# Performance work log

Measured on AMD Instinct MI355X. Metric: run time of the kernel, lower is better.

The kernel has to match this reference:

```python
import jax, jax.numpy as jnp
import numpy as np

H = 256   # hidden_dim
K = 4     # number of z_layer Linears
T = 8192  # number of permutation trees (Z-nodes) in the batch
C = 16    # children (leaf indices) per tree
N = 200000  # rows in batch.x node-feature table


def setup_inputs() -> dict:
    key = jax.random.key(0)
    ks = jax.random.split(key, 6)
    x = jax.random.normal(ks[0], (N, H), dtype=jnp.float32)
    leaf_idx = jax.random.randint(ks[1], (T, C), 0, N)
    # z_layer: k Linears (y = x @ W + b), z_final_layer: one Linear
    scale = 1.0 / np.sqrt(H)
    Wz = jax.random.uniform(ks[2], (K, H, H), dtype=jnp.float32, minval=-scale, maxval=scale)
    bz = jax.random.uniform(ks[3], (K, H), dtype=jnp.float32, minval=-scale, maxval=scale)
    Wzf = jax.random.uniform(ks[4], (H, H), dtype=jnp.float32, minval=-scale, maxval=scale)
    bzf = jax.random.uniform(ks[5], (H,), dtype=jnp.float32, minval=-scale, maxval=scale)
    return {"x": x, "Wz": Wz, "bz": bz, "Wzf": Wzf, "bzf": bzf, "leaf_idx": leaf_idx}


def reference(x, Wz, bz, Wzf, bzf, leaf_idx):
    # Batched z_layer_fn over T trees, each a Z-node over C leaf children.
    data = x[leaf_idx]                                   # [T, C, H] gather (fetch_or_produce)
    # k parallel Linears: [K, T, C, H]
    after = jnp.einsum('tch,khd->ktcd', data, Wz) + bz[:, None, None, :]
    # embedding_k[torch.roll(arange(C), shifts=k)] == roll(embedding_k, k, axis=children)
    k = after.shape[0]
    rolled_sum = after[0]
    for i in range(1, k):  # tiny fixed loop over k layers
        rolled_sum = rolled_sum + jnp.roll(after[i], i, axis=1)
    h = jax.nn.elu(rolled_sum)                           # [T, C, H]
    h = jnp.einsum('tch,hd->tcd', h, Wzf) + bzf          # z_final_layer
    out = jax.nn.elu(jnp.sum(h, axis=1))                 # sum over children, ELU -> [T, H]
    return out
```

## Files before the change

kernel.cpp:

```cpp
#include <hip/hip_runtime.h>
#include <hip/hip_bf16.h>
#include <stdint.h>

#define TREES 8192
#define HID   256
#define CH    16
#define KL    4
#define G     8
#define LDSS  264

typedef short bf16x8 __attribute__((ext_vector_type(8)));
typedef float f32x4  __attribute__((ext_vector_type(4)));

__device__ __forceinline__ unsigned short f2bf(float f) {
    unsigned u = __builtin_bit_cast(unsigned, f);
    u += 0x7FFFu + ((u >> 16) & 1u);
    return (unsigned short)(u >> 16);
}
__device__ __forceinline__ float elu1(float x) {
    return x > 0.f ? x : (__expf(x) - 1.f);
}

__global__ void prep_transpose(const float* __restrict__ Wz,
                               const float* __restrict__ Wzf,
                               unsigned short* __restrict__ WzT,
                               unsigned short* __restrict__ WzfT) {
    __shared__ unsigned short ts[64][65];
    const int k  = blockIdx.z;
    const int h0 = blockIdx.x * 64;
    const int d0 = blockIdx.y * 64;
    const float* src = (k < KL) ? (Wz + (k << 16)) : Wzf;
    unsigned short* dst = (k < KL) ? (WzT + (k << 16)) : WzfT;
    const int tid = threadIdx.x;
    const int jc  = tid & 63;
    #pragma unroll
    for (int r = 0; r < 16; ++r) {
        int i = r * 4 + (tid >> 6);
        ts[jc][i] = f2bf(src[(h0 + i) * HID + d0 + jc]);
    }
    __syncthreads();
    #pragma unroll
    for (int r = 0; r < 16; ++r) {
        int jl = r * 4 + (tid >> 6);
        dst[(d0 + jl) * HID + h0 + jc] = ts[jl][jc];
    }
}

__global__ void prep_bzsum(const float* __restrict__ bz, float* __restrict__ bzsum) {
    int d = threadIdx.x;
    float s = 0.f;
    #pragma unroll
    for (int k = 0; k < KL; ++k) s += bz[k * HID + d];
    bzsum[d] = s;
}

__global__ __launch_bounds__(256, 2) void ptree_kernel(
    const float* __restrict__ x,
    const int* __restrict__ leaf,
    const float* __restrict__ bzf,
    const unsigned short* __restrict__ WzT,
    const unsigned short* __restrict__ WzfT,
    const float* __restrict__ bzsum,
    float* __restrict__ out,
    int nrows)
{
    __shared__ __align__(16) unsigned short sh[G][CH][LDSS];
    __shared__ __align__(16) unsigned short hs[CH][LDSS];
    const int tid  = threadIdx.x;
    const int lane = tid & 63;
    const int wave = tid >> 6;
    const int t0   = blockIdx.x * G;
    const int ncol = lane & 15;
    const int quad = lane >> 4;

    #pragma unroll
    for (int i = 0; i < (G * CH * 32) / 256; ++i) {
        int cid = i * 256 + tid;
        int g   = cid >> 9;
        int row = (cid >> 5) & 15;
        int ch  = cid & 31;
        int idx = leaf[(t0 + g) * CH + row];
        idx = (idx >= 0 && idx < nrows) ? idx : 0;
        const float* src = x + (size_t)idx * HID + ch * 8;
        float4 v0 = *(const float4*)src;
        float4 v1 = *(const float4*)(src + 4);
        union { uint4 u4; unsigned short s[8]; } U;
        U.s[0] = f2bf(v0.x); U.s[1] = f2bf(v0.y);
        U.s[2] = f2bf(v0.z); U.s[3] = f2bf(v0.w);
        U.s[4] = f2bf(v1.x); U.s[5] = f2bf(v1.y);
        U.s[6] = f2bf(v1.z); U.s[7] = f2bf(v1.w);
        *(uint4*)&sh[g][row][ch * 8] = U.u4;
    }

    float bzs[4], bzfv[4];
    #pragma unroll
    for (int nt = 0; nt < 4; ++nt) {
        bzs[nt]  = bzsum[wave * 64 + nt * 16 + ncol];
        bzfv[nt] = bzf[wave * 64 + nt * 16 + ncol];
    }

    __syncthreads();

    f32x4 acc1[G][4];
    #pragma unroll
    for (int g = 0; g < G; ++g)
        #pragma unroll
        for (int nt = 0; nt < 4; ++nt) acc1[g][nt] = f32x4{0.f, 0.f, 0.f, 0.f};

    const unsigned short* wz_base = WzT + (wave * 64 + ncol) * HID + quad * 8;
    bf16x8 bc[4], bn[4];
    #pragma unroll
    for (int nt = 0; nt < 4; ++nt)
        bc[nt] = *(const bf16x8*)(wz_base + nt * 16 * HID);

    #pragma unroll 2
    for (int s = 0; s < KL * 8; ++s) {
        const int sn = (s < KL * 8 - 1) ? s + 1 : s;
        const unsigned short* pn = wz_base + (sn >> 3) * 65536 + (sn & 7) * 32;
        #pragma unroll
        for (int nt = 0; nt < 4; ++nt)
            bn[nt] = *(const bf16x8*)(pn + nt * 16 * HID);
        const int k    = s >> 3;
        const int kt   = s & 7;
        const int arow = (ncol - k) & 15;
        #pragma unroll
        for (int g = 0; g < G; ++g) {
            bf16x8 a = *(const bf16x8*)&sh[g][arow][kt * 32 + quad * 8];
            #pragma unroll
            for (int nt = 0; nt < 4; ++nt)
                acc1[g][nt] = __builtin_amdgcn_mfma_f32_16x16x32_bf16(a, bc[nt], acc1[g][nt], 0, 0, 0);
        }
        #pragma unroll
        for (int nt = 0; nt < 4; ++nt) bc[nt] = bn[nt];
    }

    #pragma unroll
    for (int g = 0; g < G; ++g)
        #pragma unroll
        for (int nt = 0; nt < 4; ++nt) {
            float s = 0.f;
            #pragma unroll
            for (int r = 0; r < 4; ++r) s += elu1(acc1[g][nt][r] + bzs[nt]);
            s += __shfl_xor(s, 16);
            s += __shfl_xor(s, 32);
            if (quad == 0) hs[g][wave * 64 + nt * 16 + ncol] = f2bf(s);
        }

    __syncthreads();

    f32x4 acc2[4];
    #pragma unroll
    for (int nt = 0; nt < 4; ++nt) acc2[nt] = f32x4{0.f, 0.f, 0.f, 0.f};

    const unsigned short* wzf_base = WzfT + (wave * 64 + ncol) * HID + quad * 8;
    #pragma unroll 2
    for (int kt = 0; kt < 8; ++kt) {
        bf16x8 a = *(const bf16x8*)&hs[ncol & 7][kt * 32 + quad * 8];
        if (ncol >= 8) a = bf16x8{0, 0, 0, 0, 0, 0, 0, 0};
        #pragma unroll
        for (int nt = 0; nt < 4; ++nt) {
            bf16x8 b = *(const bf16x8*)(wzf_base + nt * 16 * HID + kt * 32);
            acc2[nt] = __builtin_amdgcn_mfma_f32_16x16x32_bf16(a, b, acc2[nt], 0, 0, 0);
        }
    }

    #pragma unroll
    for (int nt = 0; nt < 4; ++nt)
        #pragma unroll
        for (int r = 0; r < 4; ++r) {
            int tree = quad * 4 + r;
            if (tree < G) {
                float v = elu1(acc2[nt][r] + 16.f * bzfv[nt]);
                out[(size_t)(t0 + tree) * HID + wave * 64 + nt * 16 + ncol] = v;
            }
        }
}

extern "C" void kernel_launch(void* const* d_in, const int* in_sizes, int n_in,
                              void* d_out, int out_size, void* d_ws, size_t ws_size,
                              hipStream_t stream) {
    (void)out_size; (void)ws_size;
    const void* p_x = nullptr; const void* p_Wz = nullptr; const void* p_bz = nullptr;
    const void* p_Wzf = nullptr; const void* p_bzf = nullptr; const void* p_leaf = nullptr;
    for (int i = 0; i < n_in; ++i) {
        switch (in_sizes[i]) {
            case 200000 * 256:   p_x    = d_in[i]; break;
            case KL * 256 * 256: p_Wz   = d_in[i]; break;
            case KL * 256:       p_bz   = d_in[i]; break;
            case 256 * 256:      p_Wzf  = d_in[i]; break;
            case 256:            p_bzf  = d_in[i]; break;
            case TREES * CH:     p_leaf = d_in[i]; break;
        }
    }
    const float* x    = (const float*)p_x;
    const float* Wz   = (const float*)p_Wz;
    const float* bz   = (const float*)p_bz;
    const float* Wzf  = (const float*)p_Wzf;
    const float* bzf  = (const float*)p_bzf;
    const int*   leaf = (const int*)p_leaf;

    unsigned short* WzT  = (unsigned short*)d_ws;
    unsigned short* WzfT = WzT + KL * HID * HID;
    float*          bzsum = (float*)(WzfT + HID * HID);

    dim3 tg(4, 4, KL + 1);
    prep_transpose<<<tg, 256, 0, stream>>>(Wz, Wzf, WzT, WzfT);
    prep_bzsum<<<1, HID, 0, stream>>>(bz, bzsum);
    ptree_kernel<<<TREES / G, 256, 0, stream>>>(x, leaf, bzf, WzT, WzfT, bzsum,
                                                (float*)d_out, 200000);
}
```

Measured before the change: 350.4 us.

## Double-buffer gathered leaf rows across tree chunks and fuse bias-sum prep

Each block now handles 16 trees in four chunks of four. The next chunk's x rows are gathered into registers while the current chunk runs its MFMAs, then written into a second LDS buffer. This is meant to hide the random-gather latency behind compute and to fill all 16 rows of the final MFMA, where the old code zeroed half of them. The bz-sum kernel is folded into the transpose prep kernel, saving one launch. The cost is higher register pressure from the prefetch buffers and fewer, longer blocks (512 instead of 1024).

```diff
diff --git a/kernel.cpp b/kernel.cpp
--- a/kernel.cpp
+++ b/kernel.cpp
@@ -1,12 +1,13 @@
 #include <hip/hip_runtime.h>
-#include <hip/hip_bf16.h>
 #include <stdint.h>
 
 #define TREES 8192
 #define HID   256
 #define CH    16
 #define KL    4
-#define G     8
+#define GB    16
+#define CKT   4
+#define NC    (GB / CKT)
 #define LDSS  264
 
 typedef short bf16x8 __attribute__((ext_vector_type(8)));
@@ -20,11 +21,19 @@
 __device__ __forceinline__ float elu1(float x) {
     return x > 0.f ? x : (__expf(x) - 1.f);
 }
+__device__ __forceinline__ uint4 pack8(float4 a, float4 b) {
+    union { uint4 u4; unsigned short s[8]; } U;
+    U.s[0] = f2bf(a.x); U.s[1] = f2bf(a.y); U.s[2] = f2bf(a.z); U.s[3] = f2bf(a.w);
+    U.s[4] = f2bf(b.x); U.s[5] = f2bf(b.y); U.s[6] = f2bf(b.z); U.s[7] = f2bf(b.w);
+    return U.u4;
+}
 
 __global__ void prep_transpose(const float* __restrict__ Wz,
                                const float* __restrict__ Wzf,
+                               const float* __restrict__ bz,
                                unsigned short* __restrict__ WzT,
-                               unsigned short* __restrict__ WzfT) {
+                               unsigned short* __restrict__ WzfT,
+                               float* __restrict__ bzsum) {
     __shared__ unsigned short ts[64][65];
     const int k  = blockIdx.z;
     const int h0 = blockIdx.x * 64;
@@ -44,14 +53,12 @@
         int jl = r * 4 + (tid >> 6);
         dst[(d0 + jl) * HID + h0 + jc] = ts[jl][jc];
     }
-}
-
-__global__ void prep_bzsum(const float* __restrict__ bz, float* __restrict__ bzsum) {
-    int d = threadIdx.x;
-    float s = 0.f;
-    #pragma unroll
-    for (int k = 0; k < KL; ++k) s += bz[k * HID + d];
-    bzsum[d] = s;
+    if (k == KL && blockIdx.x == 0 && blockIdx.y == 0) {
+        float s = 0.f;
+        #pragma unroll
+        for (int kk = 0; kk < KL; ++kk) s += bz[kk * HID + tid];
+        bzsum[tid] = s;
+    }
 }
 
 __global__ __launch_bounds__(256, 2) void ptree_kernel(
@@ -64,32 +71,33 @@
     float* __restrict__ out,
     int nrows)
 {
-    __shared__ __align__(16) unsigned short sh[G][CH][LDSS];
-    __shared__ __align__(16) unsigned short hs[CH][LDSS];
+    __shared__ __align__(16) unsigned short sh[2][CKT][CH][LDSS];
+    __shared__ __align__(16) unsigned short hs[GB][LDSS];
     const int tid  = threadIdx.x;
     const int lane = tid & 63;
     const int wave = tid >> 6;
-    const int t0   = blockIdx.x * G;
+    const int t0   = blockIdx.x * GB;
     const int ncol = lane & 15;
     const int quad = lane >> 4;
-
-    #pragma unroll
-    for (int i = 0; i < (G * CH * 32) / 256; ++i) {
-        int cid = i * 256 + tid;
-        int g   = cid >> 9;
-        int row = (cid >> 5) & 15;
-        int ch  = cid & 31;
+    const int ch   = tid & 31;
+    const int q5   = tid >> 5;
+
+    #pragma unroll
+    for (int i = 0; i < 8; ++i) {
+        const int g = i >> 1, row = ((i & 1) << 3) + q5;
         int idx = leaf[(t0 + g) * CH + row];
-        idx = (idx >= 0 && idx < nrows) ? idx : 0;
+        idx = ((unsigned)idx < (unsigned)nrows) ? idx : 0;
         const float* src = x + (size_t)idx * HID + ch * 8;
         float4 v0 = *(const float4*)src;
         float4 v1 = *(const float4*)(src + 4);
-        union { uint4 u4; unsigned short s[8]; } U;
-        U.s[0] = f2bf(v0.x); U.s[1] = f2bf(v0.y);
-        U.s[2] = f2bf(v0.z); U.s[3] = f2bf(v0.w);
-        U.s[4] = f2bf(v1.x); U.s[5] = f2bf(v1.y);
-        U.s[6] = f2bf(v1.z); U.s[7] = f2bf(v1.w);
-        *(uint4*)&sh[g][row][ch * 8] = U.u4;
+        *(uint4*)&sh[0][g][row][ch * 8] = pack8(v0, v1);
+    }
+    int idxp[8];
+    #pragma unroll
+    for (int i = 0; i < 8; ++i) {
+        const int g = i >> 1, row = ((i & 1) << 3) + q5;
+        int idx = leaf[(t0 + CKT + g) * CH + row];
+        idxp[i] = ((unsigned)idx < (unsigned)nrows) ? idx : 0;
     }
 
     float bzs[4], bzfv[4];
@@ -99,64 +107,113 @@
         bzfv[nt] = bzf[wave * 64 + nt * 16 + ncol];
     }
 
+    const unsigned short* wz_base = WzT + (wave * 64 + ncol) * HID + quad * 8;
+    bf16x8 bp[2][4];
+    #pragma unroll
+    for (int s = 0; s < 2; ++s) {
+        const unsigned short* p = wz_base + (s >> 3) * 65536 + (s & 7) * 32;
+        #pragma unroll
+        for (int nt = 0; nt < 4; ++nt) bp[s][nt] = *(const bf16x8*)(p + nt * 16 * HID);
+    }
+
     __syncthreads();
 
-    f32x4 acc1[G][4];
-    #pragma unroll
-    for (int g = 0; g < G; ++g)
-        #pragma unroll
-        for (int nt = 0; nt < 4; ++nt) acc1[g][nt] = f32x4{0.f, 0.f, 0.f, 0.f};
-
-    const unsigned short* wz_base = WzT + (wave * 64 + ncol) * HID + quad * 8;
-    bf16x8 bc[4], bn[4];
-    #pragma unroll
-    for (int nt = 0; nt < 4; ++nt)
-        bc[nt] = *(const bf16x8*)(wz_base + nt * 16 * HID);
-
-    #pragma unroll 2
-    for (int s = 0; s < KL * 8; ++s) {
-        const int sn = (s < KL * 8 - 1) ? s + 1 : s;
-        const unsigned short* pn = wz_base + (sn >> 3) * 65536 + (sn & 7) * 32;
-        #pragma unroll
-        for (int nt = 0; nt < 4; ++nt)
-            bn[nt] = *(const bf16x8*)(pn + nt * 16 * HID);
-        const int k    = s >> 3;
-        const int kt   = s & 7;
-        const int arow = (ncol - k) & 15;
-        #pragma unroll
-        for (int g = 0; g < G; ++g) {
-            bf16x8 a = *(const bf16x8*)&sh[g][arow][kt * 32 + quad * 8];
-            #pragma unroll
-            for (int nt = 0; nt < 4; ++nt)
-                acc1[g][nt] = __builtin_amdgcn_mfma_f32_16x16x32_bf16(a, bc[nt], acc1[g][nt], 0, 0, 0);
-        }
-        #pragma unroll
-        for (int nt = 0; nt < 4; ++nt) bc[nt] = bn[nt];
-    }
-
-    #pragma unroll
-    for (int g = 0; g < G; ++g)
-        #pragma unroll
-        for (int nt = 0; nt < 4; ++nt) {
-            float s = 0.f;
-            #pragma unroll
-            for (int r = 0; r < 4; ++r) s += elu1(acc1[g][nt][r] + bzs[nt]);
-            s += __shfl_xor(s, 16);
-            s += __shfl_xor(s, 32);
-            if (quad == 0) hs[g][wave * 64 + nt * 16 + ncol] = f2bf(s);
-        }
-
-    __syncthreads();
+    for (int c = 0; c < NC; ++c) {
+        const int pb   = c & 1;
+        const int more = (c < NC - 1);
+
+        float4 xa[8], xb[8];
+        if (more) {
+            #pragma unroll
+            for (int i = 0; i < 4; ++i) {
+                const float* src = x + (size_t)idxp[i] * HID + ch * 8;
+                xa[2 * i]     = *(const float4*)src;
+                xa[2 * i + 1] = *(const float4*)(src + 4);
+            }
+        }
+
+        f32x4 acc1[CKT][4];
+        #pragma unroll
+        for (int g = 0; g < CKT; ++g)
+            #pragma unroll
+            for (int nt = 0; nt < 4; ++nt) acc1[g][nt] = f32x4{0.f, 0.f, 0.f, 0.f};
+
+        #pragma unroll
+        for (int k = 0; k < KL; ++k) {
+            if (k == 1 && more) {
+                #pragma unroll
+                for (int i = 4; i < 8; ++i) {
+                    const float* src = x + (size_t)idxp[i] * HID + ch * 8;
+                    xb[2 * (i - 4)]     = *(const float4*)src;
+                    xb[2 * (i - 4) + 1] = *(const float4*)(src + 4);
+                }
+            }
+            if (k == 2 && more) {
+                #pragma unroll
+                for (int i = 0; i < 4; ++i) {
+                    const int g = i >> 1, row = ((i & 1) << 3) + q5;
+                    *(uint4*)&sh[pb ^ 1][g][row][ch * 8] = pack8(xa[2 * i], xa[2 * i + 1]);
+                }
+                if (c + 2 < NC) {
+                    #pragma unroll
+                    for (int i = 0; i < 8; ++i) {
+                        const int g = i >> 1, row = ((i & 1) << 3) + q5;
+                        int idx = leaf[(t0 + (c + 2) * CKT + g) * CH + row];
+                        idxp[i] = ((unsigned)idx < (unsigned)nrows) ? idx : 0;
+                    }
+                }
+            }
+            if (k == 3 && more) {
+                #pragma unroll
+                for (int i = 4; i < 8; ++i) {
+                    const int g = i >> 1, row = ((i & 1) << 3) + q5;
+                    *(uint4*)&sh[pb ^ 1][g][row][ch * 8] =
+                        pack8(xb[2 * (i - 4)], xb[2 * (i - 4) + 1]);
+                }
+            }
+            const int arow = (ncol - k) & 15;
+            #pragma unroll
+            for (int kt = 0; kt < 8; ++kt) {
+                const int s = k * 8 + kt;
+                #pragma unroll
+                for (int g = 0; g < CKT; ++g) {
+                    bf16x8 a = *(const bf16x8*)&sh[pb][g][arow][kt * 32 + quad * 8];
+                    #pragma unroll
+                    for (int nt = 0; nt < 4; ++nt)
+                        acc1[g][nt] = __builtin_amdgcn_mfma_f32_16x16x32_bf16(
+                            a, bp[s & 1][nt], acc1[g][nt], 0, 0, 0);
+                }
+                const int sn = (s + 2) & 31;
+                const unsigned short* pn = wz_base + (sn >> 3) * 65536 + (sn & 7) * 32;
+                #pragma unroll
+                for (int nt = 0; nt < 4; ++nt)
+                    bp[s & 1][nt] = *(const bf16x8*)(pn + nt * 16 * HID);
+            }
+        }
+
+        #pragma unroll
+        for (int g = 0; g < CKT; ++g)
+            #pragma unroll
+            for (int nt = 0; nt < 4; ++nt) {
+                float sv = 0.f;
+                #pragma unroll
+                for (int r = 0; r < 4; ++r) sv += elu1(acc1[g][nt][r] + bzs[nt]);
+                sv += __shfl_xor(sv, 16);
+                sv += __shfl_xor(sv, 32);
+                if (quad == 0) hs[c * CKT + g][wave * 64 + nt * 16 + ncol] = f2bf(sv);
+            }
+
+        __syncthreads();
+    }
 
     f32x4 acc2[4];
     #pragma unroll
     for (int nt = 0; nt < 4; ++nt) acc2[nt] = f32x4{0.f, 0.f, 0.f, 0.f};
 
     const unsigned short* wzf_base = WzfT + (wave * 64 + ncol) * HID + quad * 8;
-    #pragma unroll 2
+    #pragma unroll
     for (int kt = 0; kt < 8; ++kt) {
-        bf16x8 a = *(const bf16x8*)&hs[ncol & 7][kt * 32 + quad * 8];
-        if (ncol >= 8) a = bf16x8{0, 0, 0, 0, 0, 0, 0, 0};
+        bf16x8 a = *(const bf16x8*)&hs[ncol][kt * 32 + quad * 8];
         #pragma unroll
         for (int nt = 0; nt < 4; ++nt) {
             bf16x8 b = *(const bf16x8*)(wzf_base + nt * 16 * HID + kt * 32);
@@ -168,11 +225,9 @@
     for (int nt = 0; nt < 4; ++nt)
         #pragma unroll
         for (int r = 0; r < 4; ++r) {
-            int tree = quad * 4 + r;
-            if (tree < G) {
-                float v = elu1(acc2[nt][r] + 16.f * bzfv[nt]);
-                out[(size_t)(t0 + tree) * HID + wave * 64 + nt * 16 + ncol] = v;
-            }
+            const int tree = quad * 4 + r;
+            float v = elu1(acc2[nt][r] + 16.f * bzfv[nt]);
+            out[(size_t)(t0 + tree) * HID + wave * 64 + nt * 16 + ncol] = v;
         }
 }
 
@@ -204,8 +259,7 @@
     float*          bzsum = (float*)(WzfT + HID * HID);
 
     dim3 tg(4, 4, KL + 1);
-    prep_transpose<<<tg, 256, 0, stream>>>(Wz, Wzf, WzT, WzfT);
-    prep_bzsum<<<1, HID, 0, stream>>>(bz, bzsum);
-    ptree_kernel<<<TREES / G, 256, 0, stream>>>(x, leaf, bzf, WzT, WzfT, bzsum,
-                                                (float*)d_out, 200000);
-}
+    prep_transpose<<<tg, 256, 0, stream>>>(Wz, Wzf, bz, WzT, WzfT, bzsum);
+    ptree_kernel<<<TREES / GB, 256, 0, stream>>>(x, leaf, bzf, WzT, WzfT, bzsum,
+                                                 (float*)d_out, 200000);
+}
```

Result: slower. 549.8 us (+56.9%).

## Halve trees per block, raise occupancy, fold bias-sum prep into transpose kernel

Applied to the files above, without the earlier changes.

Trees per block drop from 8 to 4, which shrinks LDS and accumulator registers, and the launch bound asks for 3 blocks per CU instead of 2. The aim is more concurrent blocks to hide the latency of the random-row gather from x. The bias-sum prep kernel is merged into the transpose kernel to save one launch. The manual software prefetch of weight fragments is replaced by direct loads under a larger unroll. In exchange, each weight fragment loaded from global/L2 now feeds half as many MFMAs, so weight traffic doubles, and the second GEMM wastes 12 of 16 rows.

```diff
diff --git a/kernel.cpp b/kernel.cpp
--- a/kernel.cpp
+++ b/kernel.cpp
@@ -1,12 +1,11 @@
 #include <hip/hip_runtime.h>
-#include <hip/hip_bf16.h>
 #include <stdint.h>
 
 #define TREES 8192
 #define HID   256
 #define CH    16
 #define KL    4
-#define G     8
+#define G     4
 #define LDSS  264
 
 typedef short bf16x8 __attribute__((ext_vector_type(8)));
@@ -20,11 +19,19 @@
 __device__ __forceinline__ float elu1(float x) {
     return x > 0.f ? x : (__expf(x) - 1.f);
 }
+__device__ __forceinline__ uint4 pack8(float4 a, float4 b) {
+    union { uint4 u4; unsigned short s[8]; } U;
+    U.s[0] = f2bf(a.x); U.s[1] = f2bf(a.y); U.s[2] = f2bf(a.z); U.s[3] = f2bf(a.w);
+    U.s[4] = f2bf(b.x); U.s[5] = f2bf(b.y); U.s[6] = f2bf(b.z); U.s[7] = f2bf(b.w);
+    return U.u4;
+}
 
 __global__ void prep_transpose(const float* __restrict__ Wz,
                                const float* __restrict__ Wzf,
+                               const float* __restrict__ bz,
                                unsigned short* __restrict__ WzT,
-                               unsigned short* __restrict__ WzfT) {
+                               unsigned short* __restrict__ WzfT,
+                               float* __restrict__ bzsum) {
     __shared__ unsigned short ts[64][65];
     const int k  = blockIdx.z;
     const int h0 = blockIdx.x * 64;
@@ -44,17 +51,15 @@
         int jl = r * 4 + (tid >> 6);
         dst[(d0 + jl) * HID + h0 + jc] = ts[jl][jc];
     }
-}
-
-__global__ void prep_bzsum(const float* __restrict__ bz, float* __restrict__ bzsum) {
-    int d = threadIdx.x;
-    float s = 0.f;
-    #pragma unroll
-    for (int k = 0; k < KL; ++k) s += bz[k * HID + d];
-    bzsum[d] = s;
-}
-
-__global__ __launch_bounds__(256, 2) void ptree_kernel(
+    if (k == KL && blockIdx.x == 0 && blockIdx.y == 0) {
+        float s = 0.f;
+        #pragma unroll
+        for (int kk = 0; kk < KL; ++kk) s += bz[kk * HID + tid];
+        bzsum[tid] = s;
+    }
+}
+
+__global__ __launch_bounds__(256, 3) void ptree_kernel(
     const float* __restrict__ x,
     const int* __restrict__ leaf,
     const float* __restrict__ bzf,
@@ -65,7 +70,7 @@
     int nrows)
 {
     __shared__ __align__(16) unsigned short sh[G][CH][LDSS];
-    __shared__ __align__(16) unsigned short hs[CH][LDSS];
+    __shared__ __align__(16) unsigned short hs[G][LDSS];
     const int tid  = threadIdx.x;
     const int lane = tid & 63;
     const int wave = tid >> 6;
@@ -80,16 +85,11 @@
         int row = (cid >> 5) & 15;
         int ch  = cid & 31;
         int idx = leaf[(t0 + g) * CH + row];
-        idx = (idx >= 0 && idx < nrows) ? idx : 0;
+        idx = ((unsigned)idx < (unsigned)nrows) ? idx : 0;
         const float* src = x + (size_t)idx * HID + ch * 8;
         float4 v0 = *(const float4*)src;
         float4 v1 = *(const float4*)(src + 4);
-        union { uint4 u4; unsigned short s[8]; } U;
-        U.s[0] = f2bf(v0.x); U.s[1] = f2bf(v0.y);
-        U.s[2] = f2bf(v0.z); U.s[3] = f2bf(v0.w);
-        U.s[4] = f2bf(v1.x); U.s[5] = f2bf(v1.y);
-        U.s[6] = f2bf(v1.z); U.s[7] = f2bf(v1.w);
-        *(uint4*)&sh[g][row][ch * 8] = U.u4;
+        *(uint4*)&sh[g][row][ch * 8] = pack8(v0, v1);
     }
 
     float bzs[4], bzfv[4];
@@ -108,42 +108,37 @@
         for (int nt = 0; nt < 4; ++nt) acc1[g][nt] = f32x4{0.f, 0.f, 0.f, 0.f};
 
     const unsigned short* wz_base = WzT + (wave * 64 + ncol) * HID + quad * 8;
-    bf16x8 bc[4], bn[4];
-    #pragma unroll
-    for (int nt = 0; nt < 4; ++nt)
-        bc[nt] = *(const bf16x8*)(wz_base + nt * 16 * HID);
-
-    #pragma unroll 2
+
+    #pragma unroll 4
     for (int s = 0; s < KL * 8; ++s) {
-        const int sn = (s < KL * 8 - 1) ? s + 1 : s;
-        const unsigned short* pn = wz_base + (sn >> 3) * 65536 + (sn & 7) * 32;
+        const int k  = s >> 3;
+        const int kt = s & 7;
+        const unsigned short* bp = wz_base + k * 65536 + kt * 32;
+        bf16x8 b[4];
         #pragma unroll
         for (int nt = 0; nt < 4; ++nt)
-            bn[nt] = *(const bf16x8*)(pn + nt * 16 * HID);
-        const int k    = s >> 3;
-        const int kt   = s & 7;
+            b[nt] = *(const bf16x8*)(bp + nt * 16 * HID);
         const int arow = (ncol - k) & 15;
         #pragma unroll
         for (int g = 0; g < G; ++g) {
             bf16x8 a = *(const bf16x8*)&sh[g][arow][kt * 32 + quad * 8];
             #pragma unroll
             for (int nt = 0; nt < 4; ++nt)
-                acc1[g][nt] = __builtin_amdgcn_mfma_f32_16x16x32_bf16(a, bc[nt], acc1[g][nt], 0, 0, 0);
-        }
-        #pragma unroll
-        for (int nt = 0; nt < 4; ++nt) bc[nt] = bn[nt];
+                acc1[g][nt] = __builtin_amdgcn_mfma_f32_16x16x32_bf16(
+                    a, b[nt], acc1[g][nt], 0, 0, 0);
+        }
     }
 
     #pragma unroll
     for (int g = 0; g < G; ++g)
         #pragma unroll
         for (int nt = 0; nt < 4; ++nt) {
-            float s = 0.f;
+            float sv = 0.f;
             #pragma unroll
-            for (int r = 0; r < 4; ++r) s += elu1(acc1[g][nt][r] + bzs[nt]);
-            s += __shfl_xor(s, 16);
-            s += __shfl_xor(s, 32);
-            if (quad == 0) hs[g][wave * 64 + nt * 16 + ncol] = f2bf(s);
+            for (int r = 0; r < 4; ++r) sv += elu1(acc1[g][nt][r] + bzs[nt]);
+            sv += __shfl_xor(sv, 16);
+            sv += __shfl_xor(sv, 32);
+            if (quad == 0) hs[g][wave * 64 + nt * 16 + ncol] = f2bf(sv);
         }
 
     __syncthreads();
@@ -153,10 +148,10 @@
     for (int nt = 0; nt < 4; ++nt) acc2[nt] = f32x4{0.f, 0.f, 0.f, 0.f};
 
     const unsigned short* wzf_base = WzfT + (wave * 64 + ncol) * HID + quad * 8;
-    #pragma unroll 2
+    #pragma unroll
     for (int kt = 0; kt < 8; ++kt) {
-        bf16x8 a = *(const bf16x8*)&hs[ncol & 7][kt * 32 + quad * 8];
-        if (ncol >= 8) a = bf16x8{0, 0, 0, 0, 0, 0, 0, 0};
+        bf16x8 a = *(const bf16x8*)&hs[ncol & (G - 1)][kt * 32 + quad * 8];
+        if (ncol >= G) a = bf16x8{0, 0, 0, 0, 0, 0, 0, 0};
         #pragma unroll
         for (int nt = 0; nt < 4; ++nt) {
             bf16x8 b = *(const bf16x8*)(wzf_base + nt * 16 * HID + kt * 32);
@@ -204,8 +199,7 @@
     float*          bzsum = (float*)(WzfT + HID * HID);
 
     dim3 tg(4, 4, KL + 1);
-    prep_transpose<<<tg, 256, 0, stream>>>(Wz, Wzf, WzT, WzfT);
-    prep_bzsum<<<1, HID, 0, stream>>>(bz, bzsum);
+    prep_transpose<<<tg, 256, 0, stream>>>(Wz, Wzf, bz, WzT, WzfT, bzsum);
     ptree_kernel<<<TREES / G, 256, 0, stream>>>(x, leaf, bzf, WzT, WzfT, bzsum,
                                                 (float*)d_out, 200000);
 }
```

Result: slower. 407.7 us (+16.4%).
